# Performance work log

Hardware: AMD Instinct MI355X
Metric: run time of the kernel (lower is better)

## Reference

```python
import jax, jax.numpy as jnp
import numpy as np

FILTER_K = 100  # filter_K from __init__
NUM_CLASSES = 1000


def setup_inputs() -> dict:
    key = jax.random.key(0)
    ks = jax.random.split(key, 7)
    B, Din, D, C, N = 256, 2048, 512, NUM_CLASSES, 50000
    x = jax.random.normal(ks[0], (B, Din), jnp.float32)
    Wf = jax.random.normal(ks[1], (Din, D), jnp.float32) * 0.02
    Wc = jax.random.normal(ks[2], (C, D), jnp.float32) * 0.05
    bc = jax.random.normal(ks[3], (C,), jnp.float32) * 0.01
    supports_in = jax.random.normal(ks[4], (N, D), jnp.float32)
    ent_in = jax.random.uniform(ks[5], (N,), jnp.float32)
    labels_idx = jax.random.randint(ks[6], (N,), 0, C)
    return {"x": x, "Wf": Wf, "Wc": Wc, "bc": bc,
            "supports_in": supports_in, "ent_in": ent_in, "labels_idx": labels_idx}


def _softmax_entropy(logits):
    # -(softmax * log_softmax).sum(1), computed stably in one pass
    logp = jax.nn.log_softmax(logits, axis=1)
    return -(jnp.exp(logp) * logp).sum(axis=1)


def reference(x, Wf, Wc, bc, supports_in, ent_in, labels_idx):
    C = Wc.shape[0]
    z = x @ Wf                    # featurizer: [B, D]
    p = z @ Wc.T + bc             # classifier logits: [B, C]
    yhat = jax.nn.one_hot(jnp.argmax(p, axis=1), C, dtype=z.dtype)
    ent_new = _softmax_entropy(p)
    labels_in = jax.nn.one_hot(labels_idx, C, dtype=z.dtype)

    # grow support memory
    supports = jnp.concatenate([supports_in, z], axis=0)   # [M, D]
    labels = jnp.concatenate([labels_in, yhat], axis=0)    # [M, C]
    ent = jnp.concatenate([ent_in, ent_new], axis=0)       # [M]

    # select_supports: per-class keep FILTER_K lowest-entropy entries.
    # Torch gathers a variable-size subset; equivalent fixed-shape form is a
    # boolean mask (non-selected rows contribute zero to the weights matmul).
    y = jnp.argmax(labels, axis=1)
    M = ent.shape[0]
    order = jnp.lexsort((ent, y))            # sort by class, then entropy
    y_sorted = y[order]
    # rank of each entry within its class segment
    rank = jnp.arange(M) - jnp.searchsorted(y_sorted, y_sorted, side='left')
    mask = jnp.zeros((M,), bool).at[order].set(rank < FILTER_K)
    maskf = mask.astype(z.dtype)

    # normalize supports row-wise (F.normalize, eps=1e-12), then masked matmul
    s_norm = supports / jnp.maximum(
        jnp.linalg.norm(supports, axis=1, keepdims=True), 1e-12)
    weights = (s_norm * maskf[:, None]).T @ (labels * maskf[:, None])  # [D, C]
    weights = weights / jnp.maximum(
        jnp.linalg.norm(weights, axis=0, keepdims=True), 1e-12)
    return z @ weights            # [B, C]
```

## Files before the change

kernel.cpp:

```cpp
#include <hip/hip_runtime.h>
#include <hip/hip_bf16.h>
#include <math.h>

#define BB   256
#define DIN  2048
#define DD   512
#define CC   1000
#define NN   50000
#define MM   (NN + BB)
#define FILTER_K 100
#define SLOT 512

#define SK1  16
#define SK2  8

#define Z_OFF     0
#define CNT_OFF   (Z_OFF + BB*DD)
#define ENTN_OFF  (CNT_OFF + 1024)
#define CLS_OFF   (ENTN_OFF + BB)
#define ENTS_OFF  (CLS_OFF + BB)
#define IDXS_OFF  (ENTS_OFF + CC*SLOT)
#define WN_OFF    (IDXS_OFF + CC*SLOT)
#define ZP_OFF    (WN_OFF + CC*DD)
#define PP_OFF    (ZP_OFF + SK1*BB*DD)
#define OP_OFF    (PP_OFF + SK2*BB*CC)

#define BM 64
#define BN 128
#define BK 16

__global__ __launch_bounds__(256, 2) void gemm_ab_part(
    const float* __restrict__ A, const float* __restrict__ B,
    float* __restrict__ Cp, int M, int N, int K, int klen) {
  __shared__ float As[BK][BM + 4];
  __shared__ float Bs[BK][BN + 4];
  const int tid = threadIdx.x;
  const int m0 = blockIdx.y * BM;
  const int n0 = blockIdx.x * BN;
  const int k0 = blockIdx.z * klen;
  const int ar = tid >> 2, ac = (tid & 3) * 4;
  const int br = tid >> 4, bc = (tid & 15) * 8;
  const int tm = (tid >> 4) * 4;
  const int tn = (tid & 15) * 4;
  float acc[4][8] = {};
  for (int kk = 0; kk < klen; kk += BK) {
    float4 av  = *(const float4*)&A[(size_t)(m0 + ar) * K + (k0 + kk + ac)];
    float4 bv0 = *(const float4*)&B[(size_t)(k0 + kk + br) * N + (n0 + bc)];
    float4 bv1 = *(const float4*)&B[(size_t)(k0 + kk + br) * N + (n0 + bc + 4)];
    __syncthreads();
    As[ac + 0][ar] = av.x; As[ac + 1][ar] = av.y;
    As[ac + 2][ar] = av.z; As[ac + 3][ar] = av.w;
    *(float4*)&Bs[br][bc] = bv0;
    *(float4*)&Bs[br][bc + 4] = bv1;
    __syncthreads();
#pragma unroll
    for (int q = 0; q < BK; ++q) {
      float4 a  = *(const float4*)&As[q][tm];
      float4 b0 = *(const float4*)&Bs[q][tn];
      float4 b1 = *(const float4*)&Bs[q][tn + 64];
      float aa[4] = {a.x, a.y, a.z, a.w};
      float bb[8] = {b0.x, b0.y, b0.z, b0.w, b1.x, b1.y, b1.z, b1.w};
#pragma unroll
      for (int i = 0; i < 4; ++i)
#pragma unroll
        for (int j = 0; j < 8; ++j) acc[i][j] += aa[i] * bb[j];
    }
  }
  float* Cb = Cp + (size_t)blockIdx.z * M * N;
#pragma unroll
  for (int i = 0; i < 4; ++i) {
    *(float4*)&Cb[(size_t)(m0 + tm + i) * N + (n0 + tn)] =
        make_float4(acc[i][0], acc[i][1], acc[i][2], acc[i][3]);
    *(float4*)&Cb[(size_t)(m0 + tm + i) * N + (n0 + 64 + tn)] =
        make_float4(acc[i][4], acc[i][5], acc[i][6], acc[i][7]);
  }
}

__global__ __launch_bounds__(256, 2) void gemm_abt_part(
    const float* __restrict__ A, const float* __restrict__ B,
    float* __restrict__ Cp, int M, int L, int K, int klen) {
  __shared__ float As[BK][BM + 4];
  __shared__ float Bs[BK][BN + 4];
  const int tid = threadIdx.x;
  const int m0 = blockIdx.y * BM;
  const int n0 = blockIdx.x * BN;
  const int k0 = blockIdx.z * klen;
  const int ar = tid >> 2, ac = (tid & 3) * 4;
  const int br = tid >> 2, bc = (tid & 3) * 4;
  const int tm = (tid >> 4) * 4;
  const int tn = (tid & 15) * 4;
  float acc[4][8] = {};
  for (int kk = 0; kk < klen; kk += BK) {
    float4 av = *(const float4*)&A[(size_t)(m0 + ar) * K + (k0 + kk + ac)];
    float4 bv0 = make_float4(0.f, 0.f, 0.f, 0.f);
    float4 bv1 = make_float4(0.f, 0.f, 0.f, 0.f);
    if (n0 + br < L)
      bv0 = *(const float4*)&B[(size_t)(n0 + br) * K + (k0 + kk + bc)];
    if (n0 + 64 + br < L)
      bv1 = *(const float4*)&B[(size_t)(n0 + 64 + br) * K + (k0 + kk + bc)];
    __syncthreads();
    As[ac + 0][ar] = av.x; As[ac + 1][ar] = av.y;
    As[ac + 2][ar] = av.z; As[ac + 3][ar] = av.w;
    Bs[bc + 0][br] = bv0.x; Bs[bc + 1][br] = bv0.y;
    Bs[bc + 2][br] = bv0.z; Bs[bc + 3][br] = bv0.w;
    Bs[bc + 0][br + 64] = bv1.x; Bs[bc + 1][br + 64] = bv1.y;
    Bs[bc + 2][br + 64] = bv1.z; Bs[bc + 3][br + 64] = bv1.w;
    __syncthreads();
#pragma unroll
    for (int q = 0; q < BK; ++q) {
      float4 a  = *(const float4*)&As[q][tm];
      float4 b0 = *(const float4*)&Bs[q][tn];
      float4 b1 = *(const float4*)&Bs[q][tn + 64];
      float aa[4] = {a.x, a.y, a.z, a.w};
      float bb[8] = {b0.x, b0.y, b0.z, b0.w, b1.x, b1.y, b1.z, b1.w};
#pragma unroll
      for (int i = 0; i < 4; ++i)
#pragma unroll
        for (int j = 0; j < 8; ++j) acc[i][j] += aa[i] * bb[j];
    }
  }
  float* Cb = Cp + (size_t)blockIdx.z * M * L;
#pragma unroll
  for (int i = 0; i < 4; ++i)
#pragma unroll
    for (int j = 0; j < 4; ++j) {
      int n = n0 + tn + j;
      if (n < L) Cb[(size_t)(m0 + tm + i) * L + n] = acc[i][j];
      int n2 = n0 + 64 + tn + j;
      if (n2 < L) Cb[(size_t)(m0 + tm + i) * L + n2] = acc[i][j + 4];
    }
}

template <int S>
__global__ __launch_bounds__(256) void reduce_part(
    const float* __restrict__ part, float* __restrict__ out, int n4) {
  int i = blockIdx.x * 256 + threadIdx.x;
  if (i >= n4) return;
  const float4* p4 = (const float4*)part;
  float4 a = p4[i];
#pragma unroll
  for (int s = 1; s < S; ++s) {
    float4 b = p4[(size_t)s * n4 + i];
    a.x += b.x; a.y += b.y; a.z += b.z; a.w += b.w;
  }
  ((float4*)out)[i] = a;
}

__global__ __launch_bounds__(256) void rowstats(
    const float* __restrict__ ppart, const float* __restrict__ bc,
    float* __restrict__ ent_new, int* __restrict__ cls) {
  const int b = blockIdx.x, tid = threadIdx.x;
  const int lane = tid & 63, wid = tid >> 6;
  float r[4];
  float mv = -INFINITY; int mi = 0x7fffffff;
#pragma unroll
  for (int i = 0; i < 4; ++i) {
    int c = tid + 256 * i;
    if (c < CC) {
      float v = bc[c];
#pragma unroll
      for (int s = 0; s < SK2; ++s)
        v += ppart[(size_t)s * BB * CC + (size_t)b * CC + c];
      r[i] = v;
    } else {
      r[i] = -INFINITY;
    }
    if (r[i] > mv) { mv = r[i]; mi = c; }
  }
#pragma unroll
  for (int o = 32; o > 0; o >>= 1) {
    float ov = __shfl_down(mv, o, 64);
    int oi = __shfl_down(mi, o, 64);
    if (ov > mv || (ov == mv && oi < mi)) { mv = ov; mi = oi; }
  }
  __shared__ float smv[4]; __shared__ int smi[4];
  if (lane == 0) { smv[wid] = mv; smi[wid] = mi; }
  __syncthreads();
  if (tid == 0) {
#pragma unroll
    for (int w = 1; w < 4; ++w)
      if (smv[w] > smv[0] || (smv[w] == smv[0] && smi[w] < smi[0])) {
        smv[0] = smv[w]; smi[0] = smi[w];
      }
  }
  __syncthreads();
  const float m = smv[0]; const int am = smi[0];
  float s = 0.f, t = 0.f;
#pragma unroll
  for (int i = 0; i < 4; ++i) {
    if (tid + 256 * i < CC) {
      float u = r[i] - m;
      float e = expf(u);
      s += e; t += u * e;
    }
  }
#pragma unroll
  for (int o = 32; o > 0; o >>= 1) {
    s += __shfl_down(s, o, 64);
    t += __shfl_down(t, o, 64);
  }
  __shared__ float ssum[4], tsum[4];
  if (lane == 0) { ssum[wid] = s; tsum[wid] = t; }
  __syncthreads();
  if (tid == 0) {
    float S = ssum[0] + ssum[1] + ssum[2] + ssum[3];
    float T = tsum[0] + tsum[1] + tsum[2] + tsum[3];
    ent_new[b] = logf(S) - T / S;
    cls[b] = am;
  }
}

__global__ void scatter(const int* __restrict__ labels_idx,
                        const int* __restrict__ cls,
                        const float* __restrict__ ent_in,
                        const float* __restrict__ ent_new,
                        int* __restrict__ cnt,
                        float* __restrict__ ent_s, int* __restrict__ idx_s) {
  int m = blockIdx.x * blockDim.x + threadIdx.x;
  if (m >= MM) return;
  int c; float e;
  if (m < NN) { c = labels_idx[m]; e = ent_in[m]; }
  else        { c = cls[m - NN];   e = ent_new[m - NN]; }
  int pos = atomicAdd(&cnt[c], 1);
  if (pos < SLOT) {
    ent_s[(size_t)c * SLOT + pos] = e;
    idx_s[(size_t)c * SLOT + pos] = m;
  }
}

__global__ __launch_bounds__(256) void class_weights(
    const float* __restrict__ supports_in, const float* __restrict__ z,
    const float* __restrict__ ent_s, const int* __restrict__ idx_s,
    const int* __restrict__ cnt, float* __restrict__ wn) {
  const int c = blockIdx.x, tid = threadIdx.x;
  const int lane = tid & 63, wid = tid >> 6;
  int n = cnt[c]; if (n > SLOT) n = SLOT;

  __shared__ int sel[SLOT];
  __shared__ float se[SLOT];
  __shared__ int si[SLOT];
  int seln;
  if (n <= FILTER_K) {
    seln = n;
    for (int i = tid; i < n; i += 256) sel[i] = idx_s[(size_t)c * SLOT + i];
  } else {
    for (int i = tid; i < SLOT; i += 256) {
      if (i < n) { se[i] = ent_s[(size_t)c * SLOT + i]; si[i] = idx_s[(size_t)c * SLOT + i]; }
      else       { se[i] = INFINITY;                     si[i] = 0x7fffffff; }
    }
    __syncthreads();
    for (int k = 2; k <= SLOT; k <<= 1)
      for (int j = k >> 1; j > 0; j >>= 1) {
        for (int i = tid; i < SLOT; i += 256) {
          int ixj = i ^ j;
          if (ixj > i) {
            bool up = ((i & k) == 0);
            float e1 = se[i], e2 = se[ixj];
            int i1 = si[i], i2 = si[ixj];
            bool gt = (e1 > e2) || (e1 == e2 && i1 > i2);
            if (gt == up) { se[i] = e2; se[ixj] = e1; si[i] = i2; si[ixj] = i1; }
          }
        }
        __syncthreads();
      }
    seln = FILTER_K;
    for (int i = tid; i < FILTER_K; i += 256) sel[i] = si[i];
  }
  __syncthreads();

  float4 a0 = make_float4(0.f, 0.f, 0.f, 0.f), a1 = a0;
  for (int j = wid; j < seln; j += 4) {
    int ridx = sel[j];
    const float4* p4 = (const float4*)((ridx < NN)
        ? supports_in + (size_t)ridx * DD
        : z + (size_t)(ridx - NN) * DD);
    float4 v0 = p4[lane * 2], v1 = p4[lane * 2 + 1];
    float s = v0.x * v0.x + v0.y * v0.y + v0.z * v0.z + v0.w * v0.w
            + v1.x * v1.x + v1.y * v1.y + v1.z * v1.z + v1.w * v1.w;
#pragma unroll
    for (int o = 1; o < 64; o <<= 1) s += __shfl_xor(s, o, 64);
    float sc = 1.0f / fmaxf(sqrtf(s), 1e-12f);
    a0.x += v0.x * sc; a0.y += v0.y * sc; a0.z += v0.z * sc; a0.w += v0.w * sc;
    a1.x += v1.x * sc; a1.y += v1.y * sc; a1.z += v1.z * sc; a1.w += v1.w * sc;
  }

  __shared__ float part[4][DD];
  *(float4*)&part[wid][lane * 8] = a0;
  *(float4*)&part[wid][lane * 8 + 4] = a1;
  __syncthreads();
  const int d = tid * 2;
  float2 w;
  w.x = part[0][d] + part[1][d] + part[2][d] + part[3][d];
  w.y = part[0][d + 1] + part[1][d + 1] + part[2][d + 1] + part[3][d + 1];
  float ss = w.x * w.x + w.y * w.y;
#pragma unroll
  for (int o = 1; o < 64; o <<= 1) ss += __shfl_xor(ss, o, 64);
  __shared__ float tot[4];
  if (lane == 0) tot[wid] = ss;
  __syncthreads();
  float S = tot[0] + tot[1] + tot[2] + tot[3];
  float sc = 1.0f / fmaxf(sqrtf(S), 1e-12f);
  ((float2*)(wn + (size_t)c * DD))[tid] = make_float2(w.x * sc, w.y * sc);
}

extern "C" void kernel_launch(void* const* d_in, const int* in_sizes, int n_in,
                              void* d_out, int out_size, void* d_ws, size_t ws_size,
                              hipStream_t stream) {
  (void)in_sizes; (void)n_in; (void)out_size; (void)ws_size;
  const float* x           = (const float*)d_in[0];
  const float* Wf          = (const float*)d_in[1];
  const float* Wc          = (const float*)d_in[2];
  const float* bc          = (const float*)d_in[3];
  const float* supports_in = (const float*)d_in[4];
  const float* ent_in      = (const float*)d_in[5];
  const int*   labels_idx  = (const int*)d_in[6];
  float* out = (float*)d_out;

  float* W = (float*)d_ws;
  float* z       = W + Z_OFF;
  int*   cnt     = (int*)(W + CNT_OFF);
  float* ent_new = W + ENTN_OFF;
  int*   cls     = (int*)(W + CLS_OFF);
  float* ent_s   = W + ENTS_OFF;
  int*   idx_s   = (int*)(W + IDXS_OFF);
  float* wn      = W + WN_OFF;
  float* zpart   = W + ZP_OFF;
  float* ppart   = W + PP_OFF;
  float* opart   = W + OP_OFF;

  hipMemsetAsync(cnt, 0, 1024 * sizeof(int), stream);

  gemm_ab_part<<<dim3(DD / BN, BB / BM, SK1), 256, 0, stream>>>(
      x, Wf, zpart, BB, DD, DIN, DIN / SK1);
  reduce_part<SK1><<<(BB * DD / 4 + 255) / 256, 256, 0, stream>>>(
      zpart, z, BB * DD / 4);

  gemm_abt_part<<<dim3((CC + BN - 1) / BN, BB / BM, SK2), 256, 0, stream>>>(
      z, Wc, ppart, BB, CC, DD, DD / SK2);
  rowstats<<<BB, 256, 0, stream>>>(ppart, bc, ent_new, cls);

  scatter<<<(MM + 255) / 256, 256, 0, stream>>>(
      labels_idx, cls, ent_in, ent_new, cnt, ent_s, idx_s);
  class_weights<<<CC, 256, 0, stream>>>(supports_in, z, ent_s, idx_s, cnt, wn);

  gemm_abt_part<<<dim3((CC + BN - 1) / BN, BB / BM, SK2), 256, 0, stream>>>(
      z, wn, opart, BB, CC, DD, DD / SK2);
  reduce_part<SK2><<<(BB * CC / 4 + 255) / 256, 256, 0, stream>>>(
      opart, out, BB * CC / 4);
}
```

Measured before the change: 238.6 us.

## Fuse whole pipeline into one cooperative persistent kernel with grid syncs

Replaces the memset and eight separate launches with a single cooperative kernel of 256 blocks. Phases are separated by grid.sync: featurizer GEMM, split-K reduce, classifier GEMM, row statistics merged with the scatter, per-class weight building, output GEMM and final reduce. The classifier and output GEMMs move to 64x64 tiles with split-K of 4, and all GEMMs now prefetch the next tile into registers. This is meant to remove per-launch overhead and intermediate kernel boundaries. In exchange the grid is fixed at 256 blocks, which limits parallelism in the class-weights phase and the GEMMs.

```diff
diff --git a/kernel.cpp b/kernel.cpp
--- a/kernel.cpp
+++ b/kernel.cpp
@@ -1,6 +1,8 @@
 #include <hip/hip_runtime.h>
-#include <hip/hip_bf16.h>
+#include <hip/hip_cooperative_groups.h>
 #include <math.h>
+
+namespace cg = cooperative_groups;
 
 #define BB   256
 #define DIN  2048
@@ -12,295 +14,319 @@
 #define SLOT 512
 
 #define SK1  16
-#define SK2  8
+#define SKP  4
 
 #define Z_OFF     0
 #define CNT_OFF   (Z_OFF + BB*DD)
-#define ENTN_OFF  (CNT_OFF + 1024)
-#define CLS_OFF   (ENTN_OFF + BB)
-#define ENTS_OFF  (CLS_OFF + BB)
+#define ENTS_OFF  (CNT_OFF + 1024)
 #define IDXS_OFF  (ENTS_OFF + CC*SLOT)
 #define WN_OFF    (IDXS_OFF + CC*SLOT)
 #define ZP_OFF    (WN_OFF + CC*DD)
 #define PP_OFF    (ZP_OFF + SK1*BB*DD)
-#define OP_OFF    (PP_OFF + SK2*BB*CC)
-
-#define BM 64
-#define BN 128
-#define BK 16
-
-__global__ __launch_bounds__(256, 2) void gemm_ab_part(
-    const float* __restrict__ A, const float* __restrict__ B,
-    float* __restrict__ Cp, int M, int N, int K, int klen) {
-  __shared__ float As[BK][BM + 4];
-  __shared__ float Bs[BK][BN + 4];
-  const int tid = threadIdx.x;
-  const int m0 = blockIdx.y * BM;
-  const int n0 = blockIdx.x * BN;
-  const int k0 = blockIdx.z * klen;
+#define OP_OFF    (PP_OFF + SKP*BB*CC)
+
+__device__ __forceinline__ void gemm_abt_dev(
+    const float* __restrict__ A, const float* __restrict__ Bm,
+    float* __restrict__ Cp, float* smem, int bid, int tid) {
+  float* As = smem;
+  float* Bs = smem + 16 * 68;
+  const int nt = bid & 15, mt = (bid >> 4) & 3, sz = bid >> 6;
+  const int m0 = mt * 64, n0 = nt * 64, k0 = sz * 128;
   const int ar = tid >> 2, ac = (tid & 3) * 4;
-  const int br = tid >> 4, bc = (tid & 15) * 8;
-  const int tm = (tid >> 4) * 4;
-  const int tn = (tid & 15) * 4;
-  float acc[4][8] = {};
-  for (int kk = 0; kk < klen; kk += BK) {
-    float4 av  = *(const float4*)&A[(size_t)(m0 + ar) * K + (k0 + kk + ac)];
-    float4 bv0 = *(const float4*)&B[(size_t)(k0 + kk + br) * N + (n0 + bc)];
-    float4 bv1 = *(const float4*)&B[(size_t)(k0 + kk + br) * N + (n0 + bc + 4)];
-    __syncthreads();
-    As[ac + 0][ar] = av.x; As[ac + 1][ar] = av.y;
-    As[ac + 2][ar] = av.z; As[ac + 3][ar] = av.w;
-    *(float4*)&Bs[br][bc] = bv0;
-    *(float4*)&Bs[br][bc + 4] = bv1;
-    __syncthreads();
-#pragma unroll
-    for (int q = 0; q < BK; ++q) {
-      float4 a  = *(const float4*)&As[q][tm];
-      float4 b0 = *(const float4*)&Bs[q][tn];
-      float4 b1 = *(const float4*)&Bs[q][tn + 64];
+  const int tm = (tid >> 4) * 4, tn = (tid & 15) * 4;
+  float acc[4][4] = {};
+  float4 av = *(const float4*)&A[(size_t)(m0 + ar) * DD + k0 + ac];
+  float4 bv = make_float4(0.f, 0.f, 0.f, 0.f);
+  if (n0 + ar < CC) bv = *(const float4*)&Bm[(size_t)(n0 + ar) * DD + k0 + ac];
+  for (int kk = 0; kk < 128; kk += 16) {
+    __syncthreads();
+    As[(ac + 0) * 68 + ar] = av.x; As[(ac + 1) * 68 + ar] = av.y;
+    As[(ac + 2) * 68 + ar] = av.z; As[(ac + 3) * 68 + ar] = av.w;
+    Bs[(ac + 0) * 68 + ar] = bv.x; Bs[(ac + 1) * 68 + ar] = bv.y;
+    Bs[(ac + 2) * 68 + ar] = bv.z; Bs[(ac + 3) * 68 + ar] = bv.w;
+    __syncthreads();
+    if (kk + 16 < 128) {
+      av = *(const float4*)&A[(size_t)(m0 + ar) * DD + k0 + kk + 16 + ac];
+      if (n0 + ar < CC)
+        bv = *(const float4*)&Bm[(size_t)(n0 + ar) * DD + k0 + kk + 16 + ac];
+    }
+#pragma unroll
+    for (int q = 0; q < 16; ++q) {
+      float4 a = *(const float4*)&As[q * 68 + tm];
+      float4 b = *(const float4*)&Bs[q * 68 + tn];
       float aa[4] = {a.x, a.y, a.z, a.w};
-      float bb[8] = {b0.x, b0.y, b0.z, b0.w, b1.x, b1.y, b1.z, b1.w};
+      float bb[4] = {b.x, b.y, b.z, b.w};
 #pragma unroll
       for (int i = 0; i < 4; ++i)
 #pragma unroll
-        for (int j = 0; j < 8; ++j) acc[i][j] += aa[i] * bb[j];
-    }
-  }
-  float* Cb = Cp + (size_t)blockIdx.z * M * N;
+        for (int j = 0; j < 4; ++j) acc[i][j] += aa[i] * bb[j];
+    }
+  }
+  float* Cb = Cp + (size_t)sz * BB * CC;
 #pragma unroll
   for (int i = 0; i < 4; ++i) {
-    *(float4*)&Cb[(size_t)(m0 + tm + i) * N + (n0 + tn)] =
-        make_float4(acc[i][0], acc[i][1], acc[i][2], acc[i][3]);
-    *(float4*)&Cb[(size_t)(m0 + tm + i) * N + (n0 + 64 + tn)] =
-        make_float4(acc[i][4], acc[i][5], acc[i][6], acc[i][7]);
+    int n = n0 + tn;
+    if (n + 3 < CC) {
+      *(float4*)&Cb[(size_t)(m0 + tm + i) * CC + n] =
+          make_float4(acc[i][0], acc[i][1], acc[i][2], acc[i][3]);
+    } else {
+#pragma unroll
+      for (int j = 0; j < 4; ++j)
+        if (n + j < CC) Cb[(size_t)(m0 + tm + i) * CC + n + j] = acc[i][j];
+    }
   }
 }
 
-__global__ __launch_bounds__(256, 2) void gemm_abt_part(
-    const float* __restrict__ A, const float* __restrict__ B,
-    float* __restrict__ Cp, int M, int L, int K, int klen) {
-  __shared__ float As[BK][BM + 4];
-  __shared__ float Bs[BK][BN + 4];
-  const int tid = threadIdx.x;
-  const int m0 = blockIdx.y * BM;
-  const int n0 = blockIdx.x * BN;
-  const int k0 = blockIdx.z * klen;
-  const int ar = tid >> 2, ac = (tid & 3) * 4;
-  const int br = tid >> 2, bc = (tid & 3) * 4;
-  const int tm = (tid >> 4) * 4;
-  const int tn = (tid & 15) * 4;
-  float acc[4][8] = {};
-  for (int kk = 0; kk < klen; kk += BK) {
-    float4 av = *(const float4*)&A[(size_t)(m0 + ar) * K + (k0 + kk + ac)];
-    float4 bv0 = make_float4(0.f, 0.f, 0.f, 0.f);
-    float4 bv1 = make_float4(0.f, 0.f, 0.f, 0.f);
-    if (n0 + br < L)
-      bv0 = *(const float4*)&B[(size_t)(n0 + br) * K + (k0 + kk + bc)];
-    if (n0 + 64 + br < L)
-      bv1 = *(const float4*)&B[(size_t)(n0 + 64 + br) * K + (k0 + kk + bc)];
-    __syncthreads();
-    As[ac + 0][ar] = av.x; As[ac + 1][ar] = av.y;
-    As[ac + 2][ar] = av.z; As[ac + 3][ar] = av.w;
-    Bs[bc + 0][br] = bv0.x; Bs[bc + 1][br] = bv0.y;
-    Bs[bc + 2][br] = bv0.z; Bs[bc + 3][br] = bv0.w;
-    Bs[bc + 0][br + 64] = bv1.x; Bs[bc + 1][br + 64] = bv1.y;
-    Bs[bc + 2][br + 64] = bv1.z; Bs[bc + 3][br + 64] = bv1.w;
-    __syncthreads();
-#pragma unroll
-    for (int q = 0; q < BK; ++q) {
-      float4 a  = *(const float4*)&As[q][tm];
-      float4 b0 = *(const float4*)&Bs[q][tn];
-      float4 b1 = *(const float4*)&Bs[q][tn + 64];
-      float aa[4] = {a.x, a.y, a.z, a.w};
-      float bb[8] = {b0.x, b0.y, b0.z, b0.w, b1.x, b1.y, b1.z, b1.w};
-#pragma unroll
-      for (int i = 0; i < 4; ++i)
-#pragma unroll
-        for (int j = 0; j < 8; ++j) acc[i][j] += aa[i] * bb[j];
-    }
-  }
-  float* Cb = Cp + (size_t)blockIdx.z * M * L;
-#pragma unroll
-  for (int i = 0; i < 4; ++i)
-#pragma unroll
-    for (int j = 0; j < 4; ++j) {
-      int n = n0 + tn + j;
-      if (n < L) Cb[(size_t)(m0 + tm + i) * L + n] = acc[i][j];
-      int n2 = n0 + 64 + tn + j;
-      if (n2 < L) Cb[(size_t)(m0 + tm + i) * L + n2] = acc[i][j + 4];
-    }
-}
-
-template <int S>
-__global__ __launch_bounds__(256) void reduce_part(
-    const float* __restrict__ part, float* __restrict__ out, int n4) {
-  int i = blockIdx.x * 256 + threadIdx.x;
-  if (i >= n4) return;
-  const float4* p4 = (const float4*)part;
-  float4 a = p4[i];
-#pragma unroll
-  for (int s = 1; s < S; ++s) {
-    float4 b = p4[(size_t)s * n4 + i];
-    a.x += b.x; a.y += b.y; a.z += b.z; a.w += b.w;
-  }
-  ((float4*)out)[i] = a;
-}
-
-__global__ __launch_bounds__(256) void rowstats(
-    const float* __restrict__ ppart, const float* __restrict__ bc,
-    float* __restrict__ ent_new, int* __restrict__ cls) {
-  const int b = blockIdx.x, tid = threadIdx.x;
+__global__ __launch_bounds__(256) void mega(
+    const float* __restrict__ x, const float* __restrict__ Wf,
+    const float* __restrict__ Wc, const float* __restrict__ bc,
+    const float* __restrict__ supports_in, const float* __restrict__ ent_in,
+    const int* __restrict__ labels_idx, float* __restrict__ out,
+    float* __restrict__ ws) {
+  cg::grid_group grid = cg::this_grid();
+  __shared__ float smem[3264];
+  const int tid = threadIdx.x, bid = blockIdx.x;
   const int lane = tid & 63, wid = tid >> 6;
-  float r[4];
-  float mv = -INFINITY; int mi = 0x7fffffff;
-#pragma unroll
-  for (int i = 0; i < 4; ++i) {
-    int c = tid + 256 * i;
-    if (c < CC) {
-      float v = bc[c];
-#pragma unroll
-      for (int s = 0; s < SK2; ++s)
-        v += ppart[(size_t)s * BB * CC + (size_t)b * CC + c];
-      r[i] = v;
-    } else {
-      r[i] = -INFINITY;
-    }
-    if (r[i] > mv) { mv = r[i]; mi = c; }
-  }
-#pragma unroll
-  for (int o = 32; o > 0; o >>= 1) {
-    float ov = __shfl_down(mv, o, 64);
-    int oi = __shfl_down(mi, o, 64);
-    if (ov > mv || (ov == mv && oi < mi)) { mv = ov; mi = oi; }
-  }
-  __shared__ float smv[4]; __shared__ int smi[4];
-  if (lane == 0) { smv[wid] = mv; smi[wid] = mi; }
-  __syncthreads();
-  if (tid == 0) {
-#pragma unroll
-    for (int w = 1; w < 4; ++w)
-      if (smv[w] > smv[0] || (smv[w] == smv[0] && smi[w] < smi[0])) {
-        smv[0] = smv[w]; smi[0] = smi[w];
-      }
-  }
-  __syncthreads();
-  const float m = smv[0]; const int am = smi[0];
-  float s = 0.f, t = 0.f;
-#pragma unroll
-  for (int i = 0; i < 4; ++i) {
-    if (tid + 256 * i < CC) {
-      float u = r[i] - m;
-      float e = expf(u);
-      s += e; t += u * e;
-    }
-  }
-#pragma unroll
-  for (int o = 32; o > 0; o >>= 1) {
-    s += __shfl_down(s, o, 64);
-    t += __shfl_down(t, o, 64);
-  }
-  __shared__ float ssum[4], tsum[4];
-  if (lane == 0) { ssum[wid] = s; tsum[wid] = t; }
-  __syncthreads();
-  if (tid == 0) {
-    float S = ssum[0] + ssum[1] + ssum[2] + ssum[3];
-    float T = tsum[0] + tsum[1] + tsum[2] + tsum[3];
-    ent_new[b] = logf(S) - T / S;
-    cls[b] = am;
-  }
-}
-
-__global__ void scatter(const int* __restrict__ labels_idx,
-                        const int* __restrict__ cls,
-                        const float* __restrict__ ent_in,
-                        const float* __restrict__ ent_new,
-                        int* __restrict__ cnt,
-                        float* __restrict__ ent_s, int* __restrict__ idx_s) {
-  int m = blockIdx.x * blockDim.x + threadIdx.x;
-  if (m >= MM) return;
-  int c; float e;
-  if (m < NN) { c = labels_idx[m]; e = ent_in[m]; }
-  else        { c = cls[m - NN];   e = ent_new[m - NN]; }
-  int pos = atomicAdd(&cnt[c], 1);
-  if (pos < SLOT) {
-    ent_s[(size_t)c * SLOT + pos] = e;
-    idx_s[(size_t)c * SLOT + pos] = m;
-  }
-}
-
-__global__ __launch_bounds__(256) void class_weights(
-    const float* __restrict__ supports_in, const float* __restrict__ z,
-    const float* __restrict__ ent_s, const int* __restrict__ idx_s,
-    const int* __restrict__ cnt, float* __restrict__ wn) {
-  const int c = blockIdx.x, tid = threadIdx.x;
-  const int lane = tid & 63, wid = tid >> 6;
-  int n = cnt[c]; if (n > SLOT) n = SLOT;
-
-  __shared__ int sel[SLOT];
-  __shared__ float se[SLOT];
-  __shared__ int si[SLOT];
-  int seln;
-  if (n <= FILTER_K) {
-    seln = n;
-    for (int i = tid; i < n; i += 256) sel[i] = idx_s[(size_t)c * SLOT + i];
-  } else {
-    for (int i = tid; i < SLOT; i += 256) {
-      if (i < n) { se[i] = ent_s[(size_t)c * SLOT + i]; si[i] = idx_s[(size_t)c * SLOT + i]; }
-      else       { se[i] = INFINITY;                     si[i] = 0x7fffffff; }
-    }
-    __syncthreads();
-    for (int k = 2; k <= SLOT; k <<= 1)
-      for (int j = k >> 1; j > 0; j >>= 1) {
+
+  float* z     = ws + Z_OFF;
+  int*   cnt   = (int*)(ws + CNT_OFF);
+  float* ent_s = ws + ENTS_OFF;
+  int*   idx_s = (int*)(ws + IDXS_OFF);
+  float* wn    = ws + WN_OFF;
+  float* zpart = ws + ZP_OFF;
+  float* ppart = ws + PP_OFF;
+  float* opart = ws + OP_OFF;
+
+  if (bid == 0)
+    for (int i = tid; i < 1024; i += 256) cnt[i] = 0;
+
+  {
+    float* As = smem;
+    float* Bs = smem + 16 * 68;
+    const int bx = bid & 3, by = (bid >> 2) & 3, bz = bid >> 4;
+    const int m0 = by * 64, n0 = bx * 128, k0 = bz * 128;
+    const int ar = tid >> 2, ac = (tid & 3) * 4;
+    const int br = tid >> 4, bcn = (tid & 15) * 8;
+    const int tm = (tid >> 4) * 4, tn = (tid & 15) * 4;
+    float acc[4][8] = {};
+    float4 av  = *(const float4*)&x[(size_t)(m0 + ar) * DIN + k0 + ac];
+    float4 bv0 = *(const float4*)&Wf[(size_t)(k0 + br) * DD + n0 + bcn];
+    float4 bv1 = *(const float4*)&Wf[(size_t)(k0 + br) * DD + n0 + bcn + 4];
+    for (int kk = 0; kk < 128; kk += 16) {
+      __syncthreads();
+      As[(ac + 0) * 68 + ar] = av.x; As[(ac + 1) * 68 + ar] = av.y;
+      As[(ac + 2) * 68 + ar] = av.z; As[(ac + 3) * 68 + ar] = av.w;
+      *(float4*)&Bs[br * 132 + bcn] = bv0;
+      *(float4*)&Bs[br * 132 + bcn + 4] = bv1;
+      __syncthreads();
+      if (kk + 16 < 128) {
+        av  = *(const float4*)&x[(size_t)(m0 + ar) * DIN + k0 + kk + 16 + ac];
+        bv0 = *(const float4*)&Wf[(size_t)(k0 + kk + 16 + br) * DD + n0 + bcn];
+        bv1 = *(const float4*)&Wf[(size_t)(k0 + kk + 16 + br) * DD + n0 + bcn + 4];
+      }
+#pragma unroll
+      for (int q = 0; q < 16; ++q) {
+        float4 a  = *(const float4*)&As[q * 68 + tm];
+        float4 b0 = *(const float4*)&Bs[q * 132 + tn];
+        float4 b1 = *(const float4*)&Bs[q * 132 + tn + 64];
+        float aa[4] = {a.x, a.y, a.z, a.w};
+        float bb[8] = {b0.x, b0.y, b0.z, b0.w, b1.x, b1.y, b1.z, b1.w};
+#pragma unroll
+        for (int i = 0; i < 4; ++i)
+#pragma unroll
+          for (int j = 0; j < 8; ++j) acc[i][j] += aa[i] * bb[j];
+      }
+    }
+    float* Cb = zpart + (size_t)bz * BB * DD;
+#pragma unroll
+    for (int i = 0; i < 4; ++i) {
+      *(float4*)&Cb[(size_t)(m0 + tm + i) * DD + n0 + tn] =
+          make_float4(acc[i][0], acc[i][1], acc[i][2], acc[i][3]);
+      *(float4*)&Cb[(size_t)(m0 + tm + i) * DD + n0 + 64 + tn] =
+          make_float4(acc[i][4], acc[i][5], acc[i][6], acc[i][7]);
+    }
+  }
+  grid.sync();
+
+  {
+    int i = bid * 256 + tid;
+    if (i < BB * DD / 4) {
+      const float4* p4 = (const float4*)zpart;
+      float4 a = p4[i];
+#pragma unroll
+      for (int s = 1; s < SK1; ++s) {
+        float4 b = p4[(size_t)s * (BB * DD / 4) + i];
+        a.x += b.x; a.y += b.y; a.z += b.z; a.w += b.w;
+      }
+      ((float4*)z)[i] = a;
+    }
+  }
+  grid.sync();
+
+  gemm_abt_dev(z, Wc, ppart, smem, bid, tid);
+  grid.sync();
+
+  {
+    const int b = bid;
+    float* smv = smem;            int* smi = (int*)(smem + 4);
+    float* ssm = smem + 8;        float* tsm = smem + 12;
+    float r[4];
+    float mv = -INFINITY; int mi = 0x7fffffff;
+#pragma unroll
+    for (int i = 0; i < 4; ++i) {
+      int c = tid + 256 * i;
+      if (c < CC) {
+        float v = bc[c];
+#pragma unroll
+        for (int s = 0; s < SKP; ++s)
+          v += ppart[(size_t)s * BB * CC + (size_t)b * CC + c];
+        r[i] = v;
+      } else r[i] = -INFINITY;
+      if (r[i] > mv) { mv = r[i]; mi = c; }
+    }
+#pragma unroll
+    for (int o = 32; o > 0; o >>= 1) {
+      float ov = __shfl_down(mv, o, 64);
+      int oi = __shfl_down(mi, o, 64);
+      if (ov > mv || (ov == mv && oi < mi)) { mv = ov; mi = oi; }
+    }
+    if (lane == 0) { smv[wid] = mv; smi[wid] = mi; }
+    __syncthreads();
+    if (tid == 0) {
+#pragma unroll
+      for (int w = 1; w < 4; ++w)
+        if (smv[w] > smv[0] || (smv[w] == smv[0] && smi[w] < smi[0])) {
+          smv[0] = smv[w]; smi[0] = smi[w];
+        }
+    }
+    __syncthreads();
+    const float m = smv[0]; const int am = smi[0];
+    float s = 0.f, t = 0.f;
+#pragma unroll
+    for (int i = 0; i < 4; ++i) {
+      if (tid + 256 * i < CC) {
+        float u = r[i] - m;
+        float e = expf(u);
+        s += e; t += u * e;
+      }
+    }
+#pragma unroll
+    for (int o = 32; o > 0; o >>= 1) {
+      s += __shfl_down(s, o, 64);
+      t += __shfl_down(t, o, 64);
+    }
+    if (lane == 0) { ssm[wid] = s; tsm[wid] = t; }
+    __syncthreads();
+    if (tid == 0) {
+      float S = ssm[0] + ssm[1] + ssm[2] + ssm[3];
+      float T = tsm[0] + tsm[1] + tsm[2] + tsm[3];
+      float ent = logf(S) - T / S;
+      int pos = atomicAdd(&cnt[am], 1);
+      if (pos < SLOT) {
+        ent_s[(size_t)am * SLOT + pos] = ent;
+        idx_s[(size_t)am * SLOT + pos] = NN + b;
+      }
+    }
+    int g = bid * 256 + tid;
+    if (g < NN) {
+      int c = labels_idx[g]; float e = ent_in[g];
+      int pos = atomicAdd(&cnt[c], 1);
+      if (pos < SLOT) {
+        ent_s[(size_t)c * SLOT + pos] = e;
+        idx_s[(size_t)c * SLOT + pos] = g;
+      }
+    }
+  }
+  grid.sync();
+
+  {
+    int* sel   = (int*)smem;
+    float* se  = smem + 512;
+    int* si    = (int*)(smem + 1024);
+    float* part = smem + 512;
+    float* tot  = smem + 2560;
+    for (int c = bid; c < CC; c += 256) {
+      __syncthreads();
+      int n = cnt[c]; if (n > SLOT) n = SLOT;
+      int seln;
+      if (n <= FILTER_K) {
+        seln = n;
+        for (int i = tid; i < n; i += 256) sel[i] = idx_s[(size_t)c * SLOT + i];
+      } else {
         for (int i = tid; i < SLOT; i += 256) {
-          int ixj = i ^ j;
-          if (ixj > i) {
-            bool up = ((i & k) == 0);
-            float e1 = se[i], e2 = se[ixj];
-            int i1 = si[i], i2 = si[ixj];
-            bool gt = (e1 > e2) || (e1 == e2 && i1 > i2);
-            if (gt == up) { se[i] = e2; se[ixj] = e1; si[i] = i2; si[ixj] = i1; }
-          }
+          if (i < n) { se[i] = ent_s[(size_t)c * SLOT + i]; si[i] = idx_s[(size_t)c * SLOT + i]; }
+          else       { se[i] = INFINITY;                     si[i] = 0x7fffffff; }
         }
         __syncthreads();
-      }
-    seln = FILTER_K;
-    for (int i = tid; i < FILTER_K; i += 256) sel[i] = si[i];
-  }
-  __syncthreads();
-
-  float4 a0 = make_float4(0.f, 0.f, 0.f, 0.f), a1 = a0;
-  for (int j = wid; j < seln; j += 4) {
-    int ridx = sel[j];
-    const float4* p4 = (const float4*)((ridx < NN)
-        ? supports_in + (size_t)ridx * DD
-        : z + (size_t)(ridx - NN) * DD);
-    float4 v0 = p4[lane * 2], v1 = p4[lane * 2 + 1];
-    float s = v0.x * v0.x + v0.y * v0.y + v0.z * v0.z + v0.w * v0.w
-            + v1.x * v1.x + v1.y * v1.y + v1.z * v1.z + v1.w * v1.w;
-#pragma unroll
-    for (int o = 1; o < 64; o <<= 1) s += __shfl_xor(s, o, 64);
-    float sc = 1.0f / fmaxf(sqrtf(s), 1e-12f);
-    a0.x += v0.x * sc; a0.y += v0.y * sc; a0.z += v0.z * sc; a0.w += v0.w * sc;
-    a1.x += v1.x * sc; a1.y += v1.y * sc; a1.z += v1.z * sc; a1.w += v1.w * sc;
-  }
-
-  __shared__ float part[4][DD];
-  *(float4*)&part[wid][lane * 8] = a0;
-  *(float4*)&part[wid][lane * 8 + 4] = a1;
-  __syncthreads();
-  const int d = tid * 2;
-  float2 w;
-  w.x = part[0][d] + part[1][d] + part[2][d] + part[3][d];
-  w.y = part[0][d + 1] + part[1][d + 1] + part[2][d + 1] + part[3][d + 1];
-  float ss = w.x * w.x + w.y * w.y;
-#pragma unroll
-  for (int o = 1; o < 64; o <<= 1) ss += __shfl_xor(ss, o, 64);
-  __shared__ float tot[4];
-  if (lane == 0) tot[wid] = ss;
-  __syncthreads();
-  float S = tot[0] + tot[1] + tot[2] + tot[3];
-  float sc = 1.0f / fmaxf(sqrtf(S), 1e-12f);
-  ((float2*)(wn + (size_t)c * DD))[tid] = make_float2(w.x * sc, w.y * sc);
+        for (int k = 2; k <= SLOT; k <<= 1)
+          for (int j = k >> 1; j > 0; j >>= 1) {
+            for (int i = tid; i < SLOT; i += 256) {
+              int ixj = i ^ j;
+              if (ixj > i) {
+                bool up = ((i & k) == 0);
+                float e1 = se[i], e2 = se[ixj];
+                int i1 = si[i], i2 = si[ixj];
+                bool gt = (e1 > e2) || (e1 == e2 && i1 > i2);
+                if (gt == up) { se[i] = e2; se[ixj] = e1; si[i] = i2; si[ixj] = i1; }
+              }
+            }
+            __syncthreads();
+          }
+        seln = FILTER_K;
+        for (int i = tid; i < FILTER_K; i += 256) sel[i] = si[i];
+      }
+      __syncthreads();
+
+      float4 a0 = make_float4(0.f, 0.f, 0.f, 0.f), a1 = a0;
+      for (int j = wid; j < seln; j += 4) {
+        int ridx = sel[j];
+        const float4* p4 = (const float4*)((ridx < NN)
+            ? supports_in + (size_t)ridx * DD
+            : z + (size_t)(ridx - NN) * DD);
+        float4 v0 = p4[lane * 2], v1 = p4[lane * 2 + 1];
+        float s = v0.x * v0.x + v0.y * v0.y + v0.z * v0.z + v0.w * v0.w
+                + v1.x * v1.x + v1.y * v1.y + v1.z * v1.z + v1.w * v1.w;
+#pragma unroll
+        for (int o = 1; o < 64; o <<= 1) s += __shfl_xor(s, o, 64);
+        float sc = 1.0f / fmaxf(sqrtf(s), 1e-12f);
+        a0.x += v0.x * sc; a0.y += v0.y * sc; a0.z += v0.z * sc; a0.w += v0.w * sc;
+        a1.x += v1.x * sc; a1.y += v1.y * sc; a1.z += v1.z * sc; a1.w += v1.w * sc;
+      }
+      __syncthreads();
+      *(float4*)&part[wid * 512 + lane * 8] = a0;
+      *(float4*)&part[wid * 512 + lane * 8 + 4] = a1;
+      __syncthreads();
+      const int d = tid * 2;
+      float wx = part[d] + part[512 + d] + part[1024 + d] + part[1536 + d];
+      float wy = part[d + 1] + part[512 + d + 1] + part[1024 + d + 1] + part[1536 + d + 1];
+      float ss = wx * wx + wy * wy;
+#pragma unroll
+      for (int o = 1; o < 64; o <<= 1) ss += __shfl_xor(ss, o, 64);
+      if (lane == 0) tot[wid] = ss;
+      __syncthreads();
+      float S = tot[0] + tot[1] + tot[2] + tot[3];
+      float sc = 1.0f / fmaxf(sqrtf(S), 1e-12f);
+      ((float2*)(wn + (size_t)c * DD))[tid] = make_float2(wx * sc, wy * sc);
+    }
+  }
+  grid.sync();
+
+  gemm_abt_dev(z, wn, opart, smem, bid, tid);
+  grid.sync();
+
+  {
+    int i = bid * 256 + tid;
+    if (i < BB * CC / 4) {
+      const float4* p4 = (const float4*)opart;
+      float4 a = p4[i];
+#pragma unroll
+      for (int s = 1; s < SKP; ++s) {
+        float4 b = p4[(size_t)s * (BB * CC / 4) + i];
+        a.x += b.x; a.y += b.y; a.z += b.z; a.w += b.w;
+      }
+      ((float4*)out)[i] = a;
+    }
+  }
 }
 
 extern "C" void kernel_launch(void* const* d_in, const int* in_sizes, int n_in,
@@ -315,36 +341,11 @@
   const float* ent_in      = (const float*)d_in[5];
   const int*   labels_idx  = (const int*)d_in[6];
   float* out = (float*)d_out;
-
-  float* W = (float*)d_ws;
-  float* z       = W + Z_OFF;
-  int*   cnt     = (int*)(W + CNT_OFF);
-  float* ent_new = W + ENTN_OFF;
-  int*   cls     = (int*)(W + CLS_OFF);
-  float* ent_s   = W + ENTS_OFF;
-  int*   idx_s   = (int*)(W + IDXS_OFF);
-  float* wn      = W + WN_OFF;
-  float* zpart   = W + ZP_OFF;
-  float* ppart   = W + PP_OFF;
-  float* opart   = W + OP_OFF;
-
-  hipMemsetAsync(cnt, 0, 1024 * sizeof(int), stream);
-
-  gemm_ab_part<<<dim3(DD / BN, BB / BM, SK1), 256, 0, stream>>>(
-      x, Wf, zpart, BB, DD, DIN, DIN / SK1);
-  reduce_part<SK1><<<(BB * DD / 4 + 255) / 256, 256, 0, stream>>>(
-      zpart, z, BB * DD / 4);
-
-  gemm_abt_part<<<dim3((CC + BN - 1) / BN, BB / BM, SK2), 256, 0, stream>>>(
-      z, Wc, ppart, BB, CC, DD, DD / SK2);
-  rowstats<<<BB, 256, 0, stream>>>(ppart, bc, ent_new, cls);
-
-  scatter<<<(MM + 255) / 256, 256, 0, stream>>>(
-      labels_idx, cls, ent_in, ent_new, cnt, ent_s, idx_s);
-  class_weights<<<CC, 256, 0, stream>>>(supports_in, z, ent_s, idx_s, cnt, wn);
-
-  gemm_abt_part<<<dim3((CC + BN - 1) / BN, BB / BM, SK2), 256, 0, stream>>>(
-      z, wn, opart, BB, CC, DD, DD / SK2);
-  reduce_part<SK2><<<(BB * CC / 4 + 255) / 256, 256, 0, stream>>>(
-      opart, out, BB * CC / 4);
+  float* ws  = (float*)d_ws;
+
+  void* args[] = {(void*)&x, (void*)&Wf, (void*)&Wc, (void*)&bc,
+                  (void*)&supports_in, (void*)&ent_in, (void*)&labels_idx,
+                  (void*)&out, (void*)&ws};
+  hipLaunchCooperativeKernel((const void*)mega, dim3(256), dim3(256),
+                             args, 0, stream);
 }
```

Result: slower. 429.2 us (+79.9%).
